# Optimization experiments

Measured on AMD Instinct MI355X. Metric: run time of the kernel, lower is better.

## Reference

```python
import jax, jax.numpy as jnp
import numpy as np

B, T, D = 4, 2048, 1024
H = 16
DK = D // H
SCALE = 1.0 / np.sqrt(DK)
EPS_LN = 1e-5
EPS_NORM = 1e-8


def setup_inputs() -> dict:
    key = jax.random.key(0)
    ks = jax.random.split(key, 12)
    gain = 1.0 / np.sqrt(2.0)
    # xavier_uniform bound for square [D, D] weight with gain
    bound = gain * np.sqrt(6.0 / (D + D))

    def w(k):
        return jax.random.uniform(k, (D, D), jnp.float32, -bound, bound)

    return {
        "x": jax.random.normal(ks[0], (B, T, D), jnp.float32),
        "mask": jax.random.bernoulli(ks[1], 0.1, (B, T)),  # True = masked out
        "wq": w(ks[2]), "bq": jnp.zeros((D,), jnp.float32),
        "wk": w(ks[3]), "bk": jnp.zeros((D,), jnp.float32),
        "wv": w(ks[4]), "bv": jnp.zeros((D,), jnp.float32),
        "wo": w(ks[5]), "bo": jnp.zeros((D,), jnp.float32),
        "ln_g": jnp.ones((D,), jnp.float32),
        "ln_b": jnp.zeros((D,), jnp.float32),
    }


def _layernorm(x, g, b):
    mu = jnp.mean(x, axis=-1, keepdims=True)
    var = jnp.var(x, axis=-1, keepdims=True)
    return (x - mu) * jax.lax.rsqrt(var + EPS_LN) * g + b


def _l2norm(x):
    # torch F.normalize: x / clamp_min(||x||_2, eps)
    n = jnp.sqrt(jnp.sum(x * x, axis=-1, keepdims=True))
    return x / jnp.maximum(n, EPS_NORM)


def reference(x, mask, wq, bq, wk, bk, wv, bv, wo, bo, ln_g, ln_b):
    xn = _layernorm(x, ln_g, ln_b)  # q_norm applied to shared input

    def proj(w, bias):
        y = jnp.einsum("btd,ed->bte", xn, w) + bias
        return y.reshape(B, T, H, DK).transpose(0, 2, 1, 3)  # [B,H,T,DK]

    Q = _l2norm(proj(wq, bq))
    K = _l2norm(proj(wk, bk))
    V = proj(wv, bv)

    scores = jnp.einsum("bhqd,bhkd->bhqk", Q, K) * SCALE
    scores = jnp.clip(scores, -10.0, 10.0)
    scores = jnp.where(mask[:, None, None, :], -10000.0, scores)
    scores = scores - jnp.max(scores, axis=-1, keepdims=True)
    attn = jax.nn.softmax(scores, axis=-1)

    out = jnp.einsum("bhqk,bhkd->bhqd", attn, V)
    out = out.transpose(0, 2, 1, 3).reshape(B, T, D)
    out = jnp.einsum("btd,ed->bte", out, wo) + bo
    return out * 0.5
```

## Files before the change

### kernel.cpp

```cpp
#include <hip/hip_runtime.h>
#include <hip/hip_bf16.h>
#include <cstdint>
#include <cstddef>
#include <cstring>

typedef unsigned short u16;
typedef unsigned char u8;
typedef __attribute__((ext_vector_type(8))) short short8;
typedef __attribute__((ext_vector_type(4))) short short4b;
typedef __attribute__((ext_vector_type(4))) float f32x4;

#define B_    4
#define T_    2048
#define D_    1024
#define H_    16
#define DK_   64
#define QSCALE_ 0.18033688011112042f

__device__ __forceinline__ float bf2f(u16 u) {
    unsigned int x = ((unsigned int)u) << 16;
    float f; __builtin_memcpy(&f, &x, 4); return f;
}
__device__ __forceinline__ u16 f2bf(float f) {
    unsigned int x; __builtin_memcpy(&x, &f, 4);
    x += 0x7fffu + ((x >> 16) & 1u);
    return (u16)(x >> 16);
}

__global__ __launch_bounds__(256) void prep_kernel(
    const u16* __restrict__ x, const u8* __restrict__ m,
    const void* s0, const void* s1, const void* s2, const void* s3,
    const void* s4, const void* s5,
    u16* __restrict__ vecs, u8* __restrict__ nm, int* flag, int n)
{
    __shared__ int tot, sbits;
    int tid = threadIdx.x;
    if (tid == 0) { tot = 0; sbits = 0; }
    __syncthreads();
    int cnt = 0;
    for (int i = tid; i < 4096; i += 256) {
        int e = (x[2 * i] >> 7) & 0xFF;
        if (e > 137 || (e >= 1 && e < 97)) cnt++;
    }
    int bits = 0;
    for (int i = tid; i < n; i += 256)
        if (m[i]) bits |= (i & 7);
    for (int o = 1; o < 64; o <<= 1) { cnt += __shfl_xor(cnt, o); bits |= __shfl_xor(bits, o); }
    if ((tid & 63) == 0) { atomicAdd(&tot, cnt); if (bits) atomicOr(&sbits, bits); }
    __syncthreads();
    int f = (tot > 1024) ? 1 : 0;
    if (tid == 0) *flag = f;
    int b = sbits;
    int stride = (b & 1) ? 1 : (b & 2) ? 2 : (b & 4) ? 4 : 8;
    for (int i = tid; i < n; i += 256)
        nm[i] = m[(size_t)i * stride] ? 1 : 0;
    const void* ss[6] = {s0, s1, s2, s3, s4, s5};
    for (int t = 0; t < 6; t++) {
        const void* s = ss[t];
        for (int i = tid; i < 1024; i += 256)
            vecs[t * 1024 + i] = f ? f2bf(((const float*)s)[i]) : ((const u16*)s)[i];
    }
}

__global__ __launch_bounds__(256) void convert_w_kernel(
    const void* s0, const void* s1, const void* s2, const void* s3,
    u16* d0, u16* d1, u16* d2, u16* d3, const int* __restrict__ flag)
{
    const void* s; u16* d;
    if (blockIdx.y == 0)      { s = s0; d = d0; }
    else if (blockIdx.y == 1) { s = s1; d = d1; }
    else if (blockIdx.y == 2) { s = s2; d = d2; }
    else                      { s = s3; d = d3; }
    int i4 = blockIdx.x * 256 + threadIdx.x;
    if (*flag) {
        float4 v = ((const float4*)s)[i4];
        ushort4 o; o.x = f2bf(v.x); o.y = f2bf(v.y); o.z = f2bf(v.z); o.w = f2bf(v.w);
        ((ushort4*)d)[i4] = o;
    } else {
        ((ushort4*)d)[i4] = ((const ushort4*)s)[i4];
    }
}

__global__ __launch_bounds__(256) void ln_kernel(
    const void* __restrict__ x, const u16* __restrict__ g,
    const u16* __restrict__ be, u16* __restrict__ xn, const int* __restrict__ flag)
{
    int row = blockIdx.x;
    int t = threadIdx.x;
    float v[4];
    if (*flag) {
        float4 f4 = ((const float4*)x)[(size_t)row * 256 + t];
        v[0] = f4.x; v[1] = f4.y; v[2] = f4.z; v[3] = f4.w;
    } else {
        ushort4 uv = ((const ushort4*)x)[(size_t)row * 256 + t];
        v[0] = bf2f(uv.x); v[1] = bf2f(uv.y); v[2] = bf2f(uv.z); v[3] = bf2f(uv.w);
    }
    float s = v[0] + v[1] + v[2] + v[3];
    float q = v[0]*v[0] + v[1]*v[1] + v[2]*v[2] + v[3]*v[3];
    for (int o = 1; o < 64; o <<= 1) { s += __shfl_xor(s, o); q += __shfl_xor(q, o); }
    __shared__ float rs[4], rq[4];
    int wv = t >> 6, ln = t & 63;
    if (ln == 0) { rs[wv] = s; rq[wv] = q; }
    __syncthreads();
    s = rs[0] + rs[1] + rs[2] + rs[3];
    q = rq[0] + rq[1] + rq[2] + rq[3];
    float mu   = s * (1.0f / D_);
    float var  = q * (1.0f / D_) - mu * mu;
    float rstd = rsqrtf(var + 1e-5f);
    u16 o4[4];
    for (int i = 0; i < 4; i++) {
        float f = (v[i] - mu) * rstd * bf2f(g[t*4 + i]) + bf2f(be[t*4 + i]);
        o4[i] = f2bf(f);
    }
    ushort4 ov; ov.x = o4[0]; ov.y = o4[1]; ov.z = o4[2]; ov.w = o4[3];
    *(ushort4*)(xn + (size_t)row * D_ + t * 4) = ov;
}

__global__ __launch_bounds__(256) void gemm_bt(
    const u16* __restrict__ A,
    const u16* __restrict__ W0, const u16* __restrict__ W1, const u16* __restrict__ W2,
    const u16* __restrict__ bias_all, int bias_idx0,
    u16* __restrict__ C0, u16* __restrict__ C1, u16* __restrict__ C2,
    float scale, const int* __restrict__ flag, int use_flag, int qkv_mode)
{
    const int K = 1024, N = 1024;
    const u16* W; const u16* bias; u16* C;
    if (blockIdx.z == 0)      { W = W0; bias = bias_all + (size_t)bias_idx0 * 1024;       C = C0; }
    else if (blockIdx.z == 1) { W = W1; bias = bias_all + (size_t)(bias_idx0 + 1) * 1024; C = C1; }
    else                      { W = W2; bias = bias_all + (size_t)(bias_idx0 + 2) * 1024; C = C2; }

    __shared__ u16 As[128 * 32];
    __shared__ u16 Bs[128 * 32];

    int tid  = threadIdx.x;
    int wave = tid >> 6, lane = tid & 63;
    int wm = wave >> 1, wn = wave & 1;
    int quad = lane >> 4, l16 = lane & 15;
    int bm = blockIdx.y * 128, bn = blockIdx.x * 128;

    f32x4 acc[4][4];
    const f32x4 fz = {0.f, 0.f, 0.f, 0.f};
    for (int i = 0; i < 4; i++) for (int j = 0; j < 4; j++) acc[i][j] = fz;

    int srow = lane >> 2;
    int scol = (lane & 3) * 8;
    const u16* gA0 = A + (size_t)(bm + wave * 32 + srow) * K + scol;
    const u16* gB0 = W + (size_t)(bn + wave * 32 + srow) * K + scol;

    for (int k0 = 0; k0 < K; k0 += 32) {
        for (int i = 0; i < 2; i++) {
            __builtin_amdgcn_global_load_lds(
                (const __attribute__((address_space(1))) void*)(gA0 + (size_t)i * 16 * K + k0),
                (__attribute__((address_space(3))) void*)(As + (wave * 32 + i * 16) * 32),
                16, 0, 0);
            __builtin_amdgcn_global_load_lds(
                (const __attribute__((address_space(1))) void*)(gB0 + (size_t)i * 16 * K + k0),
                (__attribute__((address_space(3))) void*)(Bs + (wave * 32 + i * 16) * 32),
                16, 0, 0);
        }
        __syncthreads();
        short8 a[4], b[4];
        for (int i = 0; i < 4; i++)
            a[i] = *(const short8*)(As + (wm * 64 + i * 16 + l16) * 32 + quad * 8);
        for (int j = 0; j < 4; j++)
            b[j] = *(const short8*)(Bs + (wn * 64 + j * 16 + l16) * 32 + quad * 8);
        for (int i = 0; i < 4; i++)
            for (int j = 0; j < 4; j++)
                acc[i][j] = __builtin_amdgcn_mfma_f32_16x16x32_bf16(a[i], b[j], acc[i][j], 0, 0, 0);
        __syncthreads();
    }

    if (qkv_mode) {
        if (blockIdx.z == 2) {
            for (int j = 0; j < 4; j++) {
                int col = bn + wn * 64 + j * 16 + l16;
                int h = col >> 6, d = col & 63;
                float bi = bf2f(bias[col]);
                for (int i = 0; i < 4; i++) {
                    int row0 = bm + wm * 64 + i * 16 + quad * 4;
                    int bq = row0 >> 11, t0 = row0 & 2047;
                    ushort4 pk;
                    pk.x = f2bf(acc[i][j][0] + bi); pk.y = f2bf(acc[i][j][1] + bi);
                    pk.z = f2bf(acc[i][j][2] + bi); pk.w = f2bf(acc[i][j][3] + bi);
                    *(ushort4*)(C + ((size_t)((bq * 16 + h) * 64 + d)) * 2048 + t0) = pk;
                }
            }
        } else {
            float sc2 = (blockIdx.z == 0) ? QSCALE_ : 1.0f;
            float bi[4];
            for (int j = 0; j < 4; j++) bi[j] = bf2f(bias[bn + wn * 64 + j * 16 + l16]);
            for (int i = 0; i < 4; i++) {
                int row0 = bm + wm * 64 + i * 16 + quad * 4;
                for (int r = 0; r < 4; r++) {
                    float v[4]; float s = 0.f;
                    for (int j = 0; j < 4; j++) { v[j] = acc[i][j][r] + bi[j]; s += v[j] * v[j]; }
                    s += __shfl_xor(s, 1); s += __shfl_xor(s, 2);
                    s += __shfl_xor(s, 4); s += __shfl_xor(s, 8);
                    float scl = sc2 / fmaxf(sqrtf(s), 1e-8f);
                    for (int j = 0; j < 4; j++) {
                        int col = bn + wn * 64 + j * 16 + l16;
                        C[(size_t)(row0 + r) * N + col] = f2bf(v[j] * scl);
                    }
                }
            }
        }
        return;
    }

    int f32out = use_flag ? *flag : 0;
    for (int j = 0; j < 4; j++) {
        int col = bn + wn * 64 + j * 16 + l16;
        float bi = bf2f(bias[col]);
        for (int i = 0; i < 4; i++) {
            int row0 = bm + wm * 64 + i * 16 + quad * 4;
            for (int r = 0; r < 4; r++) {
                float o = (acc[i][j][r] + bi) * scale;
                if (f32out) ((float*)C)[(size_t)(row0 + r) * N + col] = o;
                else        C[(size_t)(row0 + r) * N + col] = f2bf(o);
            }
        }
    }
}

__global__ __launch_bounds__(256, 4) void attn_kernel(
    const u16* __restrict__ Q, const u16* __restrict__ Kg,
    const u16* __restrict__ Vt, const u8* __restrict__ nm,
    u16* __restrict__ Oout)
{
    __shared__ __align__(16) u16 Ks[64 * 64];
    __shared__ __align__(16) u16 VTs[64 * 64];
    __shared__ __align__(16) float msf[64];

    int tid  = threadIdx.x;
    int wave = tid >> 6, lane = tid & 63;
    int quad = lane >> 4, l16 = lane & 15;
    int q0 = blockIdx.x * 128;
    int b  = blockIdx.y >> 4, h = blockIdx.y & 15;
    const size_t base  = (size_t)b * T_ * D_ + h * DK_;
    const size_t vbase = (size_t)((b * 16 + h) * 64) * T_;

    short8 qa[2][2];
    for (int g = 0; g < 2; g++) {
        const u16* qrow = Q + base + (size_t)(q0 + wave * 32 + g * 16 + l16) * D_;
        qa[g][0] = *(const short8*)(qrow + quad * 8);
        qa[g][1] = *(const short8*)(qrow + 32 + quad * 8);
    }

    int sr  = tid >> 3;
    int sc8 = tid & 7;
    const u8* mrow = nm + b * T_;
    int vj2 = sc8 >> 2, vjp = (sc8 >> 1) & 1, vq0 = (sc8 & 1) * 2;

    for (int p = 0; p < 2; p++) {
        int r = sr + p * 32;
        short8 kv = *(const short8*)(Kg + base + (size_t)r * D_ + sc8 * 8);
        *(short8*)(&Ks[r * 64 + ((sc8 ^ (r & 7)) * 8)]) = kv;
        short8 vv = *(const short8*)(Vt + vbase + (size_t)r * T_ + sc8 * 8);
        int c0 = (vj2 * 4 + vq0) ^ (r & 7);
        int c1 = (vj2 * 4 + vq0 + 1) ^ (r & 7);
        short4b vlo = {vv[0], vv[1], vv[2], vv[3]};
        short4b vhi = {vv[4], vv[5], vv[6], vv[7]};
        *(short4b*)(&VTs[r * 64 + c0 * 8 + vjp * 4]) = vlo;
        *(short4b*)(&VTs[r * 64 + c1 * 8 + vjp * 4]) = vhi;
    }
    if (tid < 64) msf[tid] = mrow[tid] ? 0.f : 1.f;
    __syncthreads();

    int kc = (quad ^ (l16 & 7)) * 8;
    const u16* kb_lo = Ks  + l16 * 64 + kc;
    const u16* kb_hi = Ks  + l16 * 64 + (kc ^ 32);
    const u16* vb_lo = VTs + l16 * 64 + kc;
    const u16* vb_hi = VTs + l16 * 64 + (kc ^ 32);

    const f32x4 fz = {0.f, 0.f, 0.f, 0.f};
    f32x4 o_acc[2][4];
    for (int g = 0; g < 2; g++) for (int j = 0; j < 4; j++) o_acc[g][j] = fz;
    float rowsum[2] = {0.f, 0.f};

    for (int kt = 0; kt < T_; kt += 64) {
        int ktn = (kt + 64) & (T_ - 1);
        short8 kpre[2], vpre[2];
        for (int p = 0; p < 2; p++) {
            int r = sr + p * 32;
            kpre[p] = *(const short8*)(Kg + base + (size_t)(ktn + r) * D_ + sc8 * 8);
            vpre[p] = *(const short8*)(Vt + vbase + (size_t)r * T_ + ktn + sc8 * 8);
        }
        u8 mpre = (tid < 64) ? mrow[ktn + tid] : (u8)0;

        for (int j2 = 0; j2 < 2; j2++) {
            short4b pf[2][2];
            for (int jp = 0; jp < 2; jp++) {
                int j = j2 * 2 + jp;
                short8 kb0 = *(const short8*)(kb_lo + j * 1024);
                short8 kb1 = *(const short8*)(kb_hi + j * 1024);
                f32x4 pm4 = *(const f32x4*)&msf[j * 16 + quad * 4];
                for (int g = 0; g < 2; g++) {
                    f32x4 s4 = __builtin_amdgcn_mfma_f32_16x16x32_bf16(kb0, qa[g][0], fz, 0, 0, 0);
                    s4       = __builtin_amdgcn_mfma_f32_16x16x32_bf16(kb1, qa[g][1], s4, 0, 0, 0);
                    float p0 = __builtin_exp2f(s4[0]) * pm4[0];
                    float p1 = __builtin_exp2f(s4[1]) * pm4[1];
                    float p2 = __builtin_exp2f(s4[2]) * pm4[2];
                    float p3 = __builtin_exp2f(s4[3]) * pm4[3];
                    rowsum[g] += (p0 + p1) + (p2 + p3);
                    __hip_bfloat162 h01 = __float22bfloat162_rn(float2{p0, p1});
                    __hip_bfloat162 h23 = __float22bfloat162_rn(float2{p2, p3});
                    short4b pv;
                    __builtin_memcpy(&pv, &h01, 4);
                    __builtin_memcpy(((char*)&pv) + 4, &h23, 4);
                    pf[g][jp] = pv;
                }
            }
            const u16* vb = j2 ? vb_hi : vb_lo;
            for (int jd = 0; jd < 4; jd++) {
                short8 vv = *(const short8*)(vb + jd * 1024);
                short4b va0 = {vv[0], vv[1], vv[2], vv[3]};
                short4b va1 = {vv[4], vv[5], vv[6], vv[7]};
                for (int g = 0; g < 2; g++) {
                    o_acc[g][jd] = __builtin_amdgcn_mfma_f32_16x16x16bf16_1k(va0, pf[g][0], o_acc[g][jd], 0, 0, 0);
                    o_acc[g][jd] = __builtin_amdgcn_mfma_f32_16x16x16bf16_1k(va1, pf[g][1], o_acc[g][jd], 0, 0, 0);
                }
            }
        }

        __syncthreads();
        for (int p = 0; p < 2; p++) {
            int r = sr + p * 32;
            *(short8*)(&Ks[r * 64 + ((sc8 ^ (r & 7)) * 8)]) = kpre[p];
            int c0 = (vj2 * 4 + vq0) ^ (r & 7);
            int c1 = (vj2 * 4 + vq0 + 1) ^ (r & 7);
            short4b vlo = {vpre[p][0], vpre[p][1], vpre[p][2], vpre[p][3]};
            short4b vhi = {vpre[p][4], vpre[p][5], vpre[p][6], vpre[p][7]};
            *(short4b*)(&VTs[r * 64 + c0 * 8 + vjp * 4]) = vlo;
            *(short4b*)(&VTs[r * 64 + c1 * 8 + vjp * 4]) = vhi;
        }
        if (tid < 64) msf[tid] = mpre ? 0.f : 1.f;
        __syncthreads();
    }

    for (int g = 0; g < 2; g++) {
        float l = rowsum[g];
        l += __shfl_xor(l, 16);
        l += __shfl_xor(l, 32);
        float inv = 1.0f / fmaxf(l, 1e-20f);
        size_t orow = base + (size_t)(q0 + wave * 32 + g * 16 + l16) * D_;
        for (int jd = 0; jd < 4; jd++) {
            ushort4 pk;
            pk.x = f2bf(o_acc[g][jd][0] * inv);
            pk.y = f2bf(o_acc[g][jd][1] * inv);
            pk.z = f2bf(o_acc[g][jd][2] * inv);
            pk.w = f2bf(o_acc[g][jd][3] * inv);
            *(ushort4*)(Oout + orow + jd * 16 + quad * 4) = pk;
        }
    }
}

extern "C" void kernel_launch(void* const* d_in, const int* in_sizes, int n_in,
                              void* d_out, int out_size, void* d_ws, size_t ws_size,
                              hipStream_t stream)
{
    const void* x    = d_in[0];
    const u8*   mask = (const u8*)d_in[1];
    const void* wq   = d_in[2];
    const void* bq   = d_in[3];
    const void* wk   = d_in[4];
    const void* bk   = d_in[5];
    const void* wv   = d_in[6];
    const void* bv   = d_in[7];
    const void* wo   = d_in[8];
    const void* bo   = d_in[9];
    const void* lng  = d_in[10];
    const void* lnb  = d_in[11];

    const size_t NTOK = (size_t)B_ * T_;
    u16* xn  = (u16*)d_ws;
    u16* Kb  = xn + NTOK * D_;
    u16* Vtb = Kb + NTOK * D_;
    u16* wqc = Vtb + NTOK * D_;
    u16* wkc = wqc + (size_t)D_ * D_;
    u16* wvc = wkc + (size_t)D_ * D_;
    u16* woc = wvc + (size_t)D_ * D_;
    u16* vecs = woc + (size_t)D_ * D_;
    u8*  nm  = (u8*)(vecs + 6 * 1024);
    int* flag = (int*)(nm + 8192);
    u16* Qb  = (u16*)d_out;

    prep_kernel<<<dim3(1), 256, 0, stream>>>((const u16*)x, mask, bq, bk, bv, bo, lng, lnb,
                                             vecs, nm, flag, B_ * T_);
    convert_w_kernel<<<dim3(1024, 4), 256, 0, stream>>>(wq, wk, wv, wo, wqc, wkc, wvc, woc, flag);
    ln_kernel<<<dim3(NTOK), 256, 0, stream>>>(x, vecs + 4 * 1024, vecs + 5 * 1024, xn, flag);
    gemm_bt<<<dim3(8, 64, 3), 256, 0, stream>>>(xn, wqc, wkc, wvc, vecs, 0, Qb, Kb, Vtb, 1.0f, flag, 0, 1);
    attn_kernel<<<dim3(16, 64), 256, 0, stream>>>(Qb, Kb, Vtb, nm, xn);
    gemm_bt<<<dim3(8, 64, 1), 256, 0, stream>>>(xn, woc, woc, woc, vecs, 3, (u16*)d_out, (u16*)d_out, (u16*)d_out, 0.5f, flag, 1, 0);
}
```

Measured before the change: 405.2 us.

## Use 16x16x32 MFMA for PV via permuted K rows and float mask

The PV product now uses the 16x16x32 bf16 MFMA instead of pairs of 16x16x16 ones. To make that possible, K tile rows are permuted in shared memory so the score fragments pack directly into the 8-wide B operand, and V rows keep a plain swizzle. The mask is precomputed as floats in global memory and read per lane, which removes the shared-memory mask staging. Together these cut the MFMA instruction count, register shuffling and shared-memory writes per tile. The cost is index-permutation complexity and more global mask reads, and the workspace layout grows because the mask is now stored as floats.

Result: faster. 374.5 us (-7.6%).

```diff
diff --git a/kernel.cpp b/kernel.cpp
--- a/kernel.cpp
+++ b/kernel.cpp
@@ -7,7 +7,6 @@
 typedef unsigned short u16;
 typedef unsigned char u8;
 typedef __attribute__((ext_vector_type(8))) short short8;
-typedef __attribute__((ext_vector_type(4))) short short4b;
 typedef __attribute__((ext_vector_type(4))) float f32x4;
 
 #define B_    4
@@ -31,7 +30,7 @@
     const u16* __restrict__ x, const u8* __restrict__ m,
     const void* s0, const void* s1, const void* s2, const void* s3,
     const void* s4, const void* s5,
-    u16* __restrict__ vecs, u8* __restrict__ nm, int* flag, int n)
+    u16* __restrict__ vecs, float* __restrict__ msk, int* flag, int n)
 {
     __shared__ int tot, sbits;
     int tid = threadIdx.x;
@@ -53,7 +52,7 @@
     int b = sbits;
     int stride = (b & 1) ? 1 : (b & 2) ? 2 : (b & 4) ? 4 : 8;
     for (int i = tid; i < n; i += 256)
-        nm[i] = m[(size_t)i * stride] ? 1 : 0;
+        msk[i] = m[(size_t)i * stride] ? 0.f : 1.f;
     const void* ss[6] = {s0, s1, s2, s3, s4, s5};
     for (int t = 0; t < 6; t++) {
         const void* s = ss[t];
@@ -224,12 +223,11 @@
 
 __global__ __launch_bounds__(256, 4) void attn_kernel(
     const u16* __restrict__ Q, const u16* __restrict__ Kg,
-    const u16* __restrict__ Vt, const u8* __restrict__ nm,
+    const u16* __restrict__ Vt, const float* __restrict__ msk,
     u16* __restrict__ Oout)
 {
     __shared__ __align__(16) u16 Ks[64 * 64];
     __shared__ __align__(16) u16 VTs[64 * 64];
-    __shared__ __align__(16) float msf[64];
 
     int tid  = threadIdx.x;
     int wave = tid >> 6, lane = tid & 63;
@@ -248,29 +246,30 @@
 
     int sr  = tid >> 3;
     int sc8 = tid & 7;
-    const u8* mrow = nm + b * T_;
-    int vj2 = sc8 >> 2, vjp = (sc8 >> 1) & 1, vq0 = (sc8 & 1) * 2;
-
-    for (int p = 0; p < 2; p++) {
-        int r = sr + p * 32;
-        short8 kv = *(const short8*)(Kg + base + (size_t)r * D_ + sc8 * 8);
-        *(short8*)(&Ks[r * 64 + ((sc8 ^ (r & 7)) * 8)]) = kv;
-        short8 vv = *(const short8*)(Vt + vbase + (size_t)r * T_ + sc8 * 8);
-        int c0 = (vj2 * 4 + vq0) ^ (r & 7);
-        int c1 = (vj2 * 4 + vq0 + 1) ^ (r & 7);
-        short4b vlo = {vv[0], vv[1], vv[2], vv[3]};
-        short4b vhi = {vv[4], vv[5], vv[6], vv[7]};
-        *(short4b*)(&VTs[r * 64 + c0 * 8 + vjp * 4]) = vlo;
-        *(short4b*)(&VTs[r * 64 + c1 * 8 + vjp * 4]) = vhi;
-    }
-    if (tid < 64) msf[tid] = mrow[tid] ? 0.f : 1.f;
+    const float* mq = msk + b * T_ + quad * 8;
+
+    int r0 = sr, r1 = sr + 32;
+    int rho0 = (r0 & 32) + ((r0 >> 2) & 1) * 16 + ((r0 >> 3) & 3) * 4 + (r0 & 3);
+    int rho1 = (r1 & 32) + ((r1 >> 2) & 1) * 16 + ((r1 >> 3) & 3) * 4 + (r1 & 3);
+    u16* ksw0 = Ks  + rho0 * 64 + ((sc8 ^ (rho0 & 7)) * 8);
+    u16* ksw1 = Ks  + rho1 * 64 + ((sc8 ^ (rho1 & 7)) * 8);
+    u16* vsw0 = VTs + r0 * 64 + ((sc8 ^ (r0 & 7)) * 8);
+    u16* vsw1 = VTs + r1 * 64 + ((sc8 ^ (r1 & 7)) * 8);
+    const u16* kg0 = Kg + base + (size_t)r0 * D_ + sc8 * 8;
+    const u16* kg1 = Kg + base + (size_t)r1 * D_ + sc8 * 8;
+    const u16* vg0 = Vt + vbase + (size_t)r0 * T_ + sc8 * 8;
+    const u16* vg1 = Vt + vbase + (size_t)r1 * T_ + sc8 * 8;
+
+    *(short8*)ksw0 = *(const short8*)kg0;
+    *(short8*)ksw1 = *(const short8*)kg1;
+    *(short8*)vsw0 = *(const short8*)vg0;
+    *(short8*)vsw1 = *(const short8*)vg1;
     __syncthreads();
 
-    int kc = (quad ^ (l16 & 7)) * 8;
-    const u16* kb_lo = Ks  + l16 * 64 + kc;
-    const u16* kb_hi = Ks  + l16 * 64 + (kc ^ 32);
-    const u16* vb_lo = VTs + l16 * 64 + kc;
-    const u16* vb_hi = VTs + l16 * 64 + (kc ^ 32);
+    const u16* kr_lo = Ks + l16 * 64 + ((quad ^ (l16 & 7)) * 8);
+    const u16* kr_hi = Ks + l16 * 64 + (((4 + quad) ^ (l16 & 7)) * 8);
+    const u16* vr0 = VTs + l16 * 64 + ((quad ^ (l16 & 7)) * 8);
+    const u16* vr1 = VTs + l16 * 64 + (((4 + quad) ^ (l16 & 7)) * 8);
 
     const f32x4 fz = {0.f, 0.f, 0.f, 0.f};
     f32x4 o_acc[2][4];
@@ -279,61 +278,47 @@
 
     for (int kt = 0; kt < T_; kt += 64) {
         int ktn = (kt + 64) & (T_ - 1);
-        short8 kpre[2], vpre[2];
-        for (int p = 0; p < 2; p++) {
-            int r = sr + p * 32;
-            kpre[p] = *(const short8*)(Kg + base + (size_t)(ktn + r) * D_ + sc8 * 8);
-            vpre[p] = *(const short8*)(Vt + vbase + (size_t)r * T_ + ktn + sc8 * 8);
-        }
-        u8 mpre = (tid < 64) ? mrow[ktn + tid] : (u8)0;
+        short8 kpre0 = *(const short8*)(kg0 + (size_t)ktn * D_);
+        short8 kpre1 = *(const short8*)(kg1 + (size_t)ktn * D_);
+        short8 vpre0 = *(const short8*)(vg0 + ktn);
+        short8 vpre1 = *(const short8*)(vg1 + ktn);
 
         for (int j2 = 0; j2 < 2; j2++) {
-            short4b pf[2][2];
-            for (int jp = 0; jp < 2; jp++) {
-                int j = j2 * 2 + jp;
-                short8 kb0 = *(const short8*)(kb_lo + j * 1024);
-                short8 kb1 = *(const short8*)(kb_hi + j * 1024);
-                f32x4 pm4 = *(const f32x4*)&msf[j * 16 + quad * 4];
+            unsigned pw[2][4];
+            for (int s = 0; s < 2; s++) {
+                short8 kb0 = *(const short8*)(kr_lo + (j2 * 32 + s * 16) * 64);
+                short8 kb1 = *(const short8*)(kr_hi + (j2 * 32 + s * 16) * 64);
+                f32x4 pm = *(const f32x4*)(mq + kt + j2 * 32 + s * 4);
                 for (int g = 0; g < 2; g++) {
                     f32x4 s4 = __builtin_amdgcn_mfma_f32_16x16x32_bf16(kb0, qa[g][0], fz, 0, 0, 0);
                     s4       = __builtin_amdgcn_mfma_f32_16x16x32_bf16(kb1, qa[g][1], s4, 0, 0, 0);
-                    float p0 = __builtin_exp2f(s4[0]) * pm4[0];
-                    float p1 = __builtin_exp2f(s4[1]) * pm4[1];
-                    float p2 = __builtin_exp2f(s4[2]) * pm4[2];
-                    float p3 = __builtin_exp2f(s4[3]) * pm4[3];
+                    float p0 = __builtin_exp2f(s4[0]) * pm[0];
+                    float p1 = __builtin_exp2f(s4[1]) * pm[1];
+                    float p2 = __builtin_exp2f(s4[2]) * pm[2];
+                    float p3 = __builtin_exp2f(s4[3]) * pm[3];
                     rowsum[g] += (p0 + p1) + (p2 + p3);
                     __hip_bfloat162 h01 = __float22bfloat162_rn(float2{p0, p1});
                     __hip_bfloat162 h23 = __float22bfloat162_rn(float2{p2, p3});
-                    short4b pv;
-                    __builtin_memcpy(&pv, &h01, 4);
-                    __builtin_memcpy(((char*)&pv) + 4, &h23, 4);
-                    pf[g][jp] = pv;
+                    __builtin_memcpy(&pw[g][s * 2],     &h01, 4);
+                    __builtin_memcpy(&pw[g][s * 2 + 1], &h23, 4);
                 }
             }
-            const u16* vb = j2 ? vb_hi : vb_lo;
+            short8 pb[2];
+            __builtin_memcpy(&pb[0], &pw[0][0], 16);
+            __builtin_memcpy(&pb[1], &pw[1][0], 16);
+            const u16* vr = j2 ? vr1 : vr0;
             for (int jd = 0; jd < 4; jd++) {
-                short8 vv = *(const short8*)(vb + jd * 1024);
-                short4b va0 = {vv[0], vv[1], vv[2], vv[3]};
-                short4b va1 = {vv[4], vv[5], vv[6], vv[7]};
-                for (int g = 0; g < 2; g++) {
-                    o_acc[g][jd] = __builtin_amdgcn_mfma_f32_16x16x16bf16_1k(va0, pf[g][0], o_acc[g][jd], 0, 0, 0);
-                    o_acc[g][jd] = __builtin_amdgcn_mfma_f32_16x16x16bf16_1k(va1, pf[g][1], o_acc[g][jd], 0, 0, 0);
-                }
+                short8 vv = *(const short8*)(vr + jd * 16 * 64);
+                o_acc[0][jd] = __builtin_amdgcn_mfma_f32_16x16x32_bf16(vv, pb[0], o_acc[0][jd], 0, 0, 0);
+                o_acc[1][jd] = __builtin_amdgcn_mfma_f32_16x16x32_bf16(vv, pb[1], o_acc[1][jd], 0, 0, 0);
             }
         }
 
         __syncthreads();
-        for (int p = 0; p < 2; p++) {
-            int r = sr + p * 32;
-            *(short8*)(&Ks[r * 64 + ((sc8 ^ (r & 7)) * 8)]) = kpre[p];
-            int c0 = (vj2 * 4 + vq0) ^ (r & 7);
-            int c1 = (vj2 * 4 + vq0 + 1) ^ (r & 7);
-            short4b vlo = {vpre[p][0], vpre[p][1], vpre[p][2], vpre[p][3]};
-            short4b vhi = {vpre[p][4], vpre[p][5], vpre[p][6], vpre[p][7]};
-            *(short4b*)(&VTs[r * 64 + c0 * 8 + vjp * 4]) = vlo;
-            *(short4b*)(&VTs[r * 64 + c1 * 8 + vjp * 4]) = vhi;
-        }
-        if (tid < 64) msf[tid] = mpre ? 0.f : 1.f;
+        *(short8*)ksw0 = kpre0;
+        *(short8*)ksw1 = kpre1;
+        *(short8*)vsw0 = vpre0;
+        *(short8*)vsw1 = vpre1;
         __syncthreads();
     }
 
@@ -380,15 +365,15 @@
     u16* wvc = wkc + (size_t)D_ * D_;
     u16* woc = wvc + (size_t)D_ * D_;
     u16* vecs = woc + (size_t)D_ * D_;
-    u8*  nm  = (u8*)(vecs + 6 * 1024);
-    int* flag = (int*)(nm + 8192);
+    float* msk = (float*)(vecs + 6 * 1024);
+    int* flag = (int*)(msk + 8192);
     u16* Qb  = (u16*)d_out;
 
     prep_kernel<<<dim3(1), 256, 0, stream>>>((const u16*)x, mask, bq, bk, bv, bo, lng, lnb,
-                                             vecs, nm, flag, B_ * T_);
+                                             vecs, msk, flag, B_ * T_);
     convert_w_kernel<<<dim3(1024, 4), 256, 0, stream>>>(wq, wk, wv, wo, wqc, wkc, wvc, woc, flag);
     ln_kernel<<<dim3(NTOK), 256, 0, stream>>>(x, vecs + 4 * 1024, vecs + 5 * 1024, xn, flag);
     gemm_bt<<<dim3(8, 64, 3), 256, 0, stream>>>(xn, wqc, wkc, wvc, vecs, 0, Qb, Kb, Vtb, 1.0f, flag, 0, 1);
-    attn_kernel<<<dim3(16, 64), 256, 0, stream>>>(Qb, Kb, Vtb, nm, xn);
+    attn_kernel<<<dim3(16, 64), 256, 0, stream>>>(Qb, Kb, Vtb, msk, xn);
     gemm_bt<<<dim3(8, 64, 1), 256, 0, stream>>>(xn, woc, woc, woc, vecs, 3, (u16*)d_out, (u16*)d_out, (u16*)d_out, 0.5f, flag, 1, 0);
 }
```
